# Performance work log

Measured on AMD Instinct MI355X. Metric: run time of the kernel, lower is better.

Reference implementation:

```python
import jax, jax.numpy as jnp
import numpy as np

C, H, W = 3, 224, 224
P = 14  # patches per row
PS = H // P  # 16
PATCH_DIM = C * PS * PS  # 768
HIDDEN = 768


def patchify(images):
    # images: [n, c, h, w] -> [n, P*P, c*PS*PS], flatten order (c, ph, pw)
    n = images.shape[0]
    x = images.reshape(n, C, P, PS, P, PS)
    x = x.transpose(0, 2, 4, 1, 3, 5)  # [n, Pi, Pj, c, ps, ps]
    return x.reshape(n, P * P, PATCH_DIM)


def setup_inputs() -> dict:
    key = jax.random.key(0)
    k1, k2, k3 = jax.random.split(key, 3)
    images = jax.random.normal(k1, (128, C, H, W), dtype=jnp.float32)
    # nn.Linear(patch_embedding_dim, hidden_dim): weight [out, in], bias [out]
    bound = 1.0 / np.sqrt(PATCH_DIM)
    W_lin = jax.random.uniform(k2, (HIDDEN, PATCH_DIM), minval=-bound, maxval=bound, dtype=jnp.float32)
    b_lin = jax.random.uniform(k3, (HIDDEN,), minval=-bound, maxval=bound, dtype=jnp.float32)
    cls_token = jnp.ones((1, HIDDEN), dtype=jnp.float32)
    return {"images": images, "W_lin": W_lin, "b_lin": b_lin, "cls_token": cls_token}


def reference(images, W_lin, b_lin, cls_token):
    patches = patchify(images)                        # [n, 196, 768]
    hidden = jnp.einsum('npd,hd->nph', patches, W_lin) + b_lin  # [n, 196, H]
    n = images.shape[0]
    cls = jnp.broadcast_to(cls_token[None], (n, 1, HIDDEN))
    return jnp.concatenate([cls, hidden], axis=1)     # [n, 197, H]
```

## Files before the change

### kernel.cpp

```cpp
#include <hip/hip_runtime.h>
#include <cstdint>


#define PGRID 14
#define PSZ   16
#define CHN   3
#define IMGW  224
#define KDIM  768
#define NDIM  768
#define NPATCH 196

typedef short bf16x8 __attribute__((ext_vector_type(8)));
typedef short short8v __attribute__((ext_vector_type(8)));
typedef float f32x4  __attribute__((ext_vector_type(4)));

typedef __attribute__((address_space(1))) void GV;
typedef __attribute__((address_space(3))) void LV;

__device__ __forceinline__ void gload_lds16(const void* g, void* l) {
    __builtin_amdgcn_global_load_lds((GV*)g, (LV*)l, 16, 0, 0);
}

__device__ __forceinline__ short bf16rne(float f) {
    uint32_t u = __builtin_bit_cast(uint32_t, f);
    u += 0x7FFFu + ((u >> 16) & 1u);
    return (short)(u >> 16);
}

__device__ __forceinline__ short8v cvt8(float4 v0, float4 v1) {
    short8v s;
    s[0] = bf16rne(v0.x); s[1] = bf16rne(v0.y); s[2] = bf16rne(v0.z); s[3] = bf16rne(v0.w);
    s[4] = bf16rne(v1.x); s[5] = bf16rne(v1.y); s[6] = bf16rne(v1.z); s[7] = bf16rne(v1.w);
    return s;
}

__global__ __launch_bounds__(256) void prep_all(
    const float* __restrict__ img, const float* __restrict__ Wl,
    const float* __restrict__ cls, short* __restrict__ A,
    short* __restrict__ Wb, float* __restrict__ out, int n_img)
{
    const int IMG8 = n_img * (CHN * IMGW * IMGW / 8);
    const int W8   = KDIM * NDIM / 8;
    int t = blockIdx.x * 256 + threadIdx.x;

    if (t < IMG8) {
        int w8    = t % (IMGW / 8);
        int rest  = t / (IMGW / 8);
        int h     = rest % IMGW;
        int rest2 = rest / IMGW;
        int c     = rest2 % CHN;
        int im    = rest2 / CHN;

        float4 v0 = *(const float4*)(img + (long)t * 8);
        float4 v1 = *(const float4*)(img + (long)t * 8 + 4);

        int Pi = h >> 4;
        int ph = h & 15;
        int Pj = w8 >> 1;
        int pw = (w8 & 1) * 8;
        int m  = im * NPATCH + Pi * PGRID + Pj;
        int k  = (c << 8) + (ph << 4) + pw;
        *(short8v*)(A + (long)m * KDIM + k) = cvt8(v0, v1);
    } else if (t < IMG8 + W8) {
        int u = t - IMG8;
        float4 v0 = *(const float4*)(Wl + (long)u * 8);
        float4 v1 = *(const float4*)(Wl + (long)u * 8 + 4);
        *(short8v*)(Wb + (long)u * 8) = cvt8(v0, v1);
    } else {
        int u = t - IMG8 - W8;
        if (u < n_img * (NDIM / 8)) {
            int im = u / (NDIM / 8);
            int k8 = u - im * (NDIM / 8);
            float4 v0 = *(const float4*)(cls + k8 * 8);
            float4 v1 = *(const float4*)(cls + k8 * 8 + 4);
            float* dst = out + (long)im * 197 * NDIM + k8 * 8;
            *(float4*)dst = v0;
            *(float4*)(dst + 4) = v1;
        }
    }
}

__global__ __launch_bounds__(512) void vit_gemm4(
    const short* __restrict__ A, const short* __restrict__ B,
    const float* __restrict__ bias, float* __restrict__ out,
    int M, int mgroups)
{
    const int nwg = mgroups * 3;
    const int q = nwg >> 3, r = nwg & 7;
    const int xcd = blockIdx.x & 7;
    const int idx = blockIdx.x >> 3;
    const int wgid = (xcd < r ? xcd * (q + 1) : r * (q + 1) + (xcd - r) * q) + idx;
    const int g = wgid / 3;
    const int j = wgid - g * 3;
    const int m0 = g * 256;
    const int n0 = j * 256;

    __shared__ short LDS[2][32768];

    const int tid  = threadIdx.x;
    const int wid  = tid >> 6;
    const int lane = tid & 63;
    const int wr = wid >> 2;
    const int wc = wid & 3;
    const int wm = wr * 128;
    const int wn = wc * 64;
    const int wq = lane >> 4;
    const int lr = lane & 15;
    const int blk0 = ((wq)     ^ (lr & 7)) * 8;
    const int blk1 = ((wq + 4) ^ (lr & 7)) * 8;

    const int srow = tid >> 3;
    const int sk   = (tid & 7) ^ (srow & 7);
    const long abase = (long)(m0 + srow) * KDIM + sk * 8;
    const long bbase = (long)(n0 + srow) * KDIM + sk * 8;
    const int  lslot = tid * 8;

    f32x4 acc[8][4] = {};

#define STAGE(CUR, KK)                                                       \
    {                                                                        \
        _Pragma("unroll")                                                    \
        for (int l = 0; l < 4; ++l) {                                        \
            gload_lds16(A + abase + (long)l * 64 * KDIM + (KK),              \
                        &LDS[CUR][l * 4096 + lslot]);                        \
            gload_lds16(B + bbase + (long)l * 64 * KDIM + (KK),              \
                        &LDS[CUR][16384 + l * 4096 + lslot]);                \
        }                                                                    \
    }

#define COMPUTE(CUR)                                                         \
    {                                                                        \
        _Pragma("unroll")                                                    \
        for (int ks = 0; ks < 2; ++ks) {                                     \
            const int blk = ks ? blk1 : blk0;                                \
            bf16x8 a[8], b[4];                                               \
            _Pragma("unroll")                                                \
            for (int i = 0; i < 8; ++i)                                      \
                a[i] = *(const bf16x8*)(&LDS[CUR][(wm + i * 16 + lr) * 64 + blk]); \
            _Pragma("unroll")                                                \
            for (int jm = 0; jm < 4; ++jm)                                   \
                b[jm] = *(const bf16x8*)(&LDS[CUR][16384 + (wn + jm * 16 + lr) * 64 + blk]); \
            _Pragma("unroll")                                                \
            for (int i = 0; i < 8; ++i)                                      \
                _Pragma("unroll")                                            \
                for (int jm = 0; jm < 4; ++jm)                               \
                    acc[i][jm] = __builtin_amdgcn_mfma_f32_16x16x32_bf16(    \
                        a[i], b[jm], acc[i][jm], 0, 0, 0);                   \
        }                                                                    \
    }

    STAGE(0, 0)
    STAGE(1, 64)

    for (int t = 0; t < 12; ++t) {
        const int cur = t & 1;
        if (t == 11) { asm volatile("s_waitcnt vmcnt(0)" ::: "memory"); }
        else         { asm volatile("s_waitcnt vmcnt(8)" ::: "memory"); }
        __builtin_amdgcn_s_barrier();
        asm volatile("" ::: "memory");
        COMPUTE(cur)
        asm volatile("" ::: "memory");
        __builtin_amdgcn_s_barrier();
        asm volatile("" ::: "memory");
        if (t < 10) STAGE(cur, (t + 2) * 64)
    }

#undef STAGE
#undef COMPUTE

    float bv[4];
    #pragma unroll
    for (int jm = 0; jm < 4; ++jm) bv[jm] = bias[n0 + wn + jm * 16 + lr];

    #pragma unroll
    for (int i = 0; i < 8; ++i) {
        #pragma unroll
        for (int rr = 0; rr < 4; ++rr) {
            int gm = m0 + wm + i * 16 + wq * 4 + rr;
            if (gm < M) {
                int im = gm / NPATCH;
                int p  = gm - im * NPATCH;
                long orow = ((long)im * 197 + 1 + p) * (long)NDIM;
                #pragma unroll
                for (int jm = 0; jm < 4; ++jm)
                    out[orow + n0 + wn + jm * 16 + lr] = acc[i][jm][rr] + bv[jm];
            }
        }
    }
}

#define LDSTR 40
__global__ __launch_bounds__(256) void vit_gemm_fb(
    const float* __restrict__ img, const float* __restrict__ Wl,
    const float* __restrict__ bias, float* __restrict__ out, int n_img)
{
    const int M = n_img * NPATCH;
    __shared__ short As[128 * LDSTR];
    __shared__ short Bs[128 * LDSTR];
    const int tid = threadIdx.x;
    const int m0 = blockIdx.y * 128;
    const int n0 = blockIdx.x * 128;
    const int col4  = tid & 7;
    const int rbase = tid >> 3;
    long arow[4];
    for (int rr = 0; rr < 4; ++rr) {
        int m = m0 + rbase + rr * 32;
        int mm = (m < M) ? m : (M - 1);
        int im = mm / NPATCH;
        int p  = mm % NPATCH;
        int Pi = p / PGRID;
        int Pj = p % PGRID;
        arow[rr] = ((long)(im * CHN) * IMGW + Pi * PSZ) * IMGW + Pj * PSZ;
    }
    const int lane = tid & 63;
    const int wave = tid >> 6;
    const int wm = (wave & 1) * 64;
    const int wn = (wave >> 1) * 64;
    const int wq = lane >> 4;
    const int lr = lane & 15;
    f32x4 acc[4][4] = {};
    for (int k0 = 0; k0 < KDIM; k0 += 32) {
        {
            int k  = k0 + col4 * 4;
            int c  = k >> 8;
            int ph = (k >> 4) & 15;
            int pw = k & 15;
            long koff = (long)(c * IMGW + ph) * IMGW + pw;
            #pragma unroll
            for (int rr = 0; rr < 4; ++rr) {
                const float4 v = *(const float4*)(img + arow[rr] + koff);
                int row = rbase + rr * 32;
                short4 s;
                s.x = bf16rne(v.x); s.y = bf16rne(v.y);
                s.z = bf16rne(v.z); s.w = bf16rne(v.w);
                *(short4*)(&As[row * LDSTR + col4 * 4]) = s;
            }
        }
        {
            int k = k0 + col4 * 4;
            #pragma unroll
            for (int rr = 0; rr < 4; ++rr) {
                int nrow = rbase + rr * 32;
                const float4 v = *(const float4*)(Wl + (long)(n0 + nrow) * KDIM + k);
                short4 s;
                s.x = bf16rne(v.x); s.y = bf16rne(v.y);
                s.z = bf16rne(v.z); s.w = bf16rne(v.w);
                *(short4*)(&Bs[nrow * LDSTR + col4 * 4]) = s;
            }
        }
        __syncthreads();
        bf16x8 a[4], b[4];
        #pragma unroll
        for (int i = 0; i < 4; ++i)
            a[i] = *(const bf16x8*)(&As[(wm + i * 16 + lr) * LDSTR + wq * 8]);
        #pragma unroll
        for (int i = 0; i < 4; ++i)
            b[i] = *(const bf16x8*)(&Bs[(wn + i * 16 + lr) * LDSTR + wq * 8]);
        #pragma unroll
        for (int i = 0; i < 4; ++i)
            #pragma unroll
            for (int j = 0; j < 4; ++j)
                acc[i][j] = __builtin_amdgcn_mfma_f32_16x16x32_bf16(a[i], b[j], acc[i][j], 0, 0, 0);
        __syncthreads();
    }
    float bv[4];
    #pragma unroll
    for (int j = 0; j < 4; ++j) bv[j] = bias[n0 + wn + j * 16 + lr];
    #pragma unroll
    for (int i = 0; i < 4; ++i) {
        #pragma unroll
        for (int r = 0; r < 4; ++r) {
            int gm = m0 + wm + i * 16 + wq * 4 + r;
            if (gm < M) {
                int im = gm / NPATCH;
                int p  = gm % NPATCH;
                long orow = ((long)im * 197 + 1 + p) * (long)NDIM;
                #pragma unroll
                for (int j = 0; j < 4; ++j)
                    out[orow + n0 + wn + j * 16 + lr] = acc[i][j][r] + bv[j];
            }
        }
    }
}

__global__ __launch_bounds__(256) void cls_fill(
    const float* __restrict__ cls, float* __restrict__ out, int n_img)
{
    int i = blockIdx.x * 256 + threadIdx.x;
    if (i < n_img * NDIM) {
        int im = i / NDIM;
        int n  = i - im * NDIM;
        out[(long)im * 197 * NDIM + n] = cls[n];
    }
}

extern "C" void kernel_launch(void* const* d_in, const int* in_sizes, int n_in,
                              void* d_out, int out_size, void* d_ws, size_t ws_size,
                              hipStream_t stream) {
    const float* img  = (const float*)d_in[0];
    const float* Wl   = (const float*)d_in[1];
    const float* bias = (const float*)d_in[2];
    const float* cls  = (const float*)d_in[3];
    float* out = (float*)d_out;

    int n_img = in_sizes[0] / (CHN * IMGW * IMGW);
    int M = n_img * NPATCH;
    int mgroups = (M + 255) / 256;
    long Mpad = (long)mgroups * 256;

    size_t need = (size_t)(Mpad * KDIM + (long)KDIM * NDIM) * sizeof(short);
    if (ws_size >= need) {
        short* A_ws = (short*)d_ws;
        short* Wb   = A_ws + Mpad * KDIM;

        int total8 = n_img * (CHN * IMGW * IMGW / 8)
                   + KDIM * NDIM / 8
                   + n_img * (NDIM / 8);
        prep_all<<<(total8 + 255) / 256, 256, 0, stream>>>(img, Wl, cls, A_ws, Wb, out, n_img);

        int nwg = mgroups * 3;
        vit_gemm4<<<nwg, 512, 0, stream>>>(A_ws, Wb, bias, out, M, mgroups);
    } else {
        dim3 grid(NDIM / 128, (M + 127) / 128);
        vit_gemm_fb<<<grid, 256, 0, stream>>>(img, Wl, bias, out, n_img);
        int cls_elems = n_img * NDIM;
        cls_fill<<<(cls_elems + 255) / 256, 256, 0, stream>>>(cls, out, n_img);
    }
}
```

Measured before the change: 190.7 us.

## Replace LDS-staged GEMM with direct global-to-register MFMA loads and smaller N tiles

The GEMM no longer stages A/B tiles through shared memory with global_load_lds and barriers. Each wave now loads its MFMA fragments straight from global memory into registers, double-buffered over half K-steps. The tile shrinks to 256x128 with 4 waves and twice as many workgroups, which removes LDS traffic and barrier stalls. The cost is no cross-wave reuse of operands: each wave reads its own fragments with 16-byte row-strided accesses, which leans on L2/L1 caching and may raise global memory traffic.

Result: slower. 253.4 us (+32.9%).

```diff
diff --git a/kernel.cpp b/kernel.cpp
--- a/kernel.cpp
+++ b/kernel.cpp
@@ -13,13 +13,6 @@
 typedef short bf16x8 __attribute__((ext_vector_type(8)));
 typedef short short8v __attribute__((ext_vector_type(8)));
 typedef float f32x4  __attribute__((ext_vector_type(4)));
-
-typedef __attribute__((address_space(1))) void GV;
-typedef __attribute__((address_space(3))) void LV;
-
-__device__ __forceinline__ void gload_lds16(const void* g, void* l) {
-    __builtin_amdgcn_global_load_lds((GV*)g, (LV*)l, 16, 0, 0);
-}
 
 __device__ __forceinline__ short bf16rne(float f) {
     uint32_t u = __builtin_bit_cast(uint32_t, f);
@@ -80,93 +73,68 @@
     }
 }
 
-__global__ __launch_bounds__(512) void vit_gemm4(
+__global__ __launch_bounds__(256, 2) void vit_gemm6(
     const short* __restrict__ A, const short* __restrict__ B,
     const float* __restrict__ bias, float* __restrict__ out,
     int M, int mgroups)
 {
-    const int nwg = mgroups * 3;
+    const int nwg = mgroups * 6;
     const int q = nwg >> 3, r = nwg & 7;
     const int xcd = blockIdx.x & 7;
     const int idx = blockIdx.x >> 3;
     const int wgid = (xcd < r ? xcd * (q + 1) : r * (q + 1) + (xcd - r) * q) + idx;
-    const int g = wgid / 3;
-    const int j = wgid - g * 3;
+    const int g = wgid / 6;
+    const int j = wgid - g * 6;
     const int m0 = g * 256;
-    const int n0 = j * 256;
-
-    __shared__ short LDS[2][32768];
+    const int n0 = j * 128;
 
     const int tid  = threadIdx.x;
-    const int wid  = tid >> 6;
+    const int wave = tid >> 6;
     const int lane = tid & 63;
-    const int wr = wid >> 2;
-    const int wc = wid & 3;
+    const int wr = wave >> 1;
+    const int wc = wave & 1;
     const int wm = wr * 128;
     const int wn = wc * 64;
     const int wq = lane >> 4;
     const int lr = lane & 15;
-    const int blk0 = ((wq)     ^ (lr & 7)) * 8;
-    const int blk1 = ((wq + 4) ^ (lr & 7)) * 8;
-
-    const int srow = tid >> 3;
-    const int sk   = (tid & 7) ^ (srow & 7);
-    const long abase = (long)(m0 + srow) * KDIM + sk * 8;
-    const long bbase = (long)(n0 + srow) * KDIM + sk * 8;
-    const int  lslot = tid * 8;
+
+    const long arow = (long)(m0 + wm + lr) * KDIM + wq * 8;
+    const long brow = (long)(n0 + wn + lr) * KDIM + wq * 8;
 
     f32x4 acc[8][4] = {};
-
-#define STAGE(CUR, KK)                                                       \
+    bf16x8 a0[8], b0[4], a1[8], b1[4];
+
+#define LOADH(AH, BH, KOFF)                                                  \
     {                                                                        \
         _Pragma("unroll")                                                    \
-        for (int l = 0; l < 4; ++l) {                                        \
-            gload_lds16(A + abase + (long)l * 64 * KDIM + (KK),              \
-                        &LDS[CUR][l * 4096 + lslot]);                        \
-            gload_lds16(B + bbase + (long)l * 64 * KDIM + (KK),              \
-                        &LDS[CUR][16384 + l * 4096 + lslot]);                \
-        }                                                                    \
-    }
-
-#define COMPUTE(CUR)                                                         \
+        for (int i = 0; i < 8; ++i)                                          \
+            AH[i] = *(const bf16x8*)(A + arow + (long)i * 16 * KDIM + (KOFF)); \
+        _Pragma("unroll")                                                    \
+        for (int jm = 0; jm < 4; ++jm)                                       \
+            BH[jm] = *(const bf16x8*)(B + brow + (long)jm * 16 * KDIM + (KOFF)); \
+    }
+
+#define MFMAH(AH, BH)                                                        \
     {                                                                        \
         _Pragma("unroll")                                                    \
-        for (int ks = 0; ks < 2; ++ks) {                                     \
-            const int blk = ks ? blk1 : blk0;                                \
-            bf16x8 a[8], b[4];                                               \
-            _Pragma("unroll")                                                \
-            for (int i = 0; i < 8; ++i)                                      \
-                a[i] = *(const bf16x8*)(&LDS[CUR][(wm + i * 16 + lr) * 64 + blk]); \
+        for (int i = 0; i < 8; ++i)                                          \
             _Pragma("unroll")                                                \
             for (int jm = 0; jm < 4; ++jm)                                   \
-                b[jm] = *(const bf16x8*)(&LDS[CUR][16384 + (wn + jm * 16 + lr) * 64 + blk]); \
-            _Pragma("unroll")                                                \
-            for (int i = 0; i < 8; ++i)                                      \
-                _Pragma("unroll")                                            \
-                for (int jm = 0; jm < 4; ++jm)                               \
-                    acc[i][jm] = __builtin_amdgcn_mfma_f32_16x16x32_bf16(    \
-                        a[i], b[jm], acc[i][jm], 0, 0, 0);                   \
-        }                                                                    \
-    }
-
-    STAGE(0, 0)
-    STAGE(1, 64)
-
-    for (int t = 0; t < 12; ++t) {
-        const int cur = t & 1;
-        if (t == 11) { asm volatile("s_waitcnt vmcnt(0)" ::: "memory"); }
-        else         { asm volatile("s_waitcnt vmcnt(8)" ::: "memory"); }
-        __builtin_amdgcn_s_barrier();
-        asm volatile("" ::: "memory");
-        COMPUTE(cur)
-        asm volatile("" ::: "memory");
-        __builtin_amdgcn_s_barrier();
-        asm volatile("" ::: "memory");
-        if (t < 10) STAGE(cur, (t + 2) * 64)
-    }
-
-#undef STAGE
-#undef COMPUTE
+                acc[i][jm] = __builtin_amdgcn_mfma_f32_16x16x32_bf16(        \
+                    AH[i], BH[jm], acc[i][jm], 0, 0, 0);                     \
+    }
+
+    LOADH(a0, b0, 0)
+    #pragma unroll
+    for (int kt = 0; kt < 12; ++kt) {
+        LOADH(a1, b1, kt * 64 + 32)
+        MFMAH(a0, b0)
+        if (kt < 11) LOADH(a0, b0, (kt + 1) * 64)
+        MFMAH(a1, b1)
+    }
+
+#undef LOADH
+#undef MFMAH
 
     float bv[4];
     #pragma unroll
@@ -318,8 +286,8 @@
                    + n_img * (NDIM / 8);
         prep_all<<<(total8 + 255) / 256, 256, 0, stream>>>(img, Wl, cls, A_ws, Wb, out, n_img);
 
-        int nwg = mgroups * 3;
-        vit_gemm4<<<nwg, 512, 0, stream>>>(A_ws, Wb, bias, out, M, mgroups);
+        int nwg = mgroups * 6;
+        vit_gemm6<<<nwg, 256, 0, stream>>>(A_ws, Wb, bias, out, M, mgroups);
     } else {
         dim3 grid(NDIM / 128, (M + 127) / 128);
         vit_gemm_fb<<<grid, 256, 0, stream>>>(img, Wl, bias, out, n_img);
```
